# Kernel tuning notes

Measured on AMD Instinct MI355X. Metric: run time of the kernel, lower is better.

Reference implementation:

```python
import jax, jax.numpy as jnp
import numpy as np

B, I, J, C = 1, 256, 256, 128
H, D = 4, 32          # no_heads, head_dim; c_hidden = H*D = 128
INF = 1.0e9
LN_EPS = 1e-5


def setup_inputs() -> dict:
    key = jax.random.key(0)
    ks = jax.random.split(key, 8)
    x = jax.random.normal(ks[0], (B, I, J, C), dtype=jnp.float32)
    mask = (jax.random.uniform(ks[1], (B, I, J)) > 0.1).astype(jnp.float32)
    std = 0.02
    wq = std * jax.random.normal(ks[2], (H * D, C), dtype=jnp.float32)
    wk = std * jax.random.normal(ks[3], (H * D, C), dtype=jnp.float32)
    wv = std * jax.random.normal(ks[4], (H * D, C), dtype=jnp.float32)
    wb = std * jax.random.normal(ks[5], (H, C), dtype=jnp.float32)
    wo = (std / np.sqrt(2 * H)) * jax.random.normal(ks[6], (C, H * D), dtype=jnp.float32)
    wo_b = jnp.zeros((C,), dtype=jnp.float32)
    ln_g = jnp.ones((C,), dtype=jnp.float32)
    ln_b = jnp.zeros((C,), dtype=jnp.float32)
    return {"x": x, "mask": mask, "ln_g": ln_g, "ln_b": ln_b,
            "wq": wq, "wk": wk, "wv": wv, "wb": wb, "wo": wo, "wo_b": wo_b}


def reference(x, mask, ln_g, ln_b, wq, wk, wv, wb, wo, wo_b):
    # LayerNorm over channel dim
    mu = jnp.mean(x, axis=-1, keepdims=True)
    var = jnp.mean(jnp.square(x - mu), axis=-1, keepdims=True)
    xn = (x - mu) * jax.lax.rsqrt(var + LN_EPS) * ln_g + ln_b

    # QKV projections (torch Linear: y = x @ W^T), reshape to heads
    q = (xn @ wq.T).reshape(B, I, J, H, D)
    k = (xn @ wk.T).reshape(B, I, J, H, D)
    v = (xn @ wv.T).reshape(B, I, J, H, D)

    scale = 1.0 / np.sqrt(D)
    # attention within each row i over the J dimension: [B, I, H, Jq, Jk]
    scores = jnp.einsum('biqhd,bikhd->bihqk', q, k) * scale

    # triangle bias: [B, I, J, H] -> [B, I, H, Jq, 1], broadcast over keys
    tb = jnp.einsum('bijc,hc->bijh', xn, wb)
    scores = scores + jnp.swapaxes(tb, -1, -2)[..., None]

    # mask bias: inf*(mask-1) -> [B, I, 1, Jq, 1] (as in the torch code)
    scores = scores + (INF * (mask - 1.0))[:, :, None, :, None]

    attn = jax.nn.softmax(scores, axis=-1)
    out = jnp.einsum('bihqk,bikhd->biqhd', attn, v).reshape(B, I, J, H * D)
    return out @ wo.T + wo_b
```

## Files before the change

### kernel.cpp

```cpp
#include <hip/hip_runtime.h>
#include <hip/hip_bf16.h>

typedef short bf16x8 __attribute__((ext_vector_type(8)));
typedef short bf16x4 __attribute__((ext_vector_type(4)));
typedef float f32x4  __attribute__((ext_vector_type(4)));

#define NI 256
#define NJ 256
#define NC 128
#define NH 4
#define ND 32

#define WB_OFF    0
#define WO_BF_OFF 98304
#define XN_OFF    131072
#define TBM_OFF   16908288
#define OG_OFF    17956864

__device__ __forceinline__ short f2bf(float f) {
    return __builtin_bit_cast(short, __float2bfloat16(f));
}

typedef __attribute__((address_space(1))) const void gvoid_t;
typedef __attribute__((address_space(3))) void svoid_t;
__device__ __forceinline__ void load_lds16(const void* g, void* l) {
    __builtin_amdgcn_global_load_lds((gvoid_t*)g, (svoid_t*)l, 16, 0, 0);
}

__global__ __launch_bounds__(256, 8)
void k_conv(const float* __restrict__ wq, const float* __restrict__ wk,
            const float* __restrict__ wv, const float* __restrict__ wo,
            char* __restrict__ ws)
{
    const int gt = blockIdx.x * 256 + threadIdx.x;
    const int base = gt * 4;
    const float* src;
    short* dst;
    if (base < 49152) {
        const int t = base >> 14;
        src = (t == 0 ? wq : (t == 1 ? wk : wv)) + (base & 16383);
        dst = (short*)(ws + WB_OFF) + base;
    } else {
        src = wo + (base - 49152);
        dst = (short*)(ws + WO_BF_OFF) + (base - 49152);
    }
    f32x4 v = *(const f32x4*)src;
    bf16x4 o;
    #pragma unroll
    for (int r = 0; r < 4; ++r) o[r] = f2bf(v[r]);
    *(bf16x4*)dst = o;
}

__global__ __launch_bounds__(512, 4)
void k_ln(const float* __restrict__ x, const float* __restrict__ mask,
          const float* __restrict__ ln_g, const float* __restrict__ ln_b,
          const float* __restrict__ wb, char* __restrict__ ws)
{
    const int tid = threadIdx.x;
    const int t   = tid >> 2;
    const int p   = tid & 3;
    const int ch  = p * 32;
    const size_t tok = (size_t)blockIdx.x * 128 + t;

    const float* xr = x + tok * NC + ch;
    f32x4 vx[8];
    float s0 = 0.f;
    #pragma unroll
    for (int u = 0; u < 8; ++u) {
        vx[u] = *(const f32x4*)(xr + 4 * u);
        s0 += vx[u][0] + vx[u][1] + vx[u][2] + vx[u][3];
    }
    s0 += __shfl_xor(s0, 1);
    s0 += __shfl_xor(s0, 2);
    const float mu = s0 * 0.0078125f;
    float v0 = 0.f;
    #pragma unroll
    for (int u = 0; u < 8; ++u) {
        #pragma unroll
        for (int e = 0; e < 4; ++e) { float d = vx[u][e] - mu; v0 += d * d; }
    }
    v0 += __shfl_xor(v0, 1);
    v0 += __shfl_xor(v0, 2);
    const float rs = rsqrtf(v0 * 0.0078125f + 1e-5f);
    #pragma unroll
    for (int u = 0; u < 8; ++u) {
        f32x4 gg = *(const f32x4*)(ln_g + ch + 4 * u);
        f32x4 bb = *(const f32x4*)(ln_b + ch + 4 * u);
        #pragma unroll
        for (int e = 0; e < 4; ++e) vx[u][e] = (vx[u][e] - mu) * rs * gg[e] + bb[e];
    }

    float tb[4];
    #pragma unroll
    for (int h = 0; h < 4; ++h) {
        const float* wr = wb + h * NC + ch;
        float a = 0.f;
        #pragma unroll
        for (int u = 0; u < 8; ++u) {
            f32x4 w4 = *(const f32x4*)(wr + 4 * u);
            #pragma unroll
            for (int e = 0; e < 4; ++e) a += vx[u][e] * w4[e];
        }
        a += __shfl_xor(a, 1);
        a += __shfl_xor(a, 2);
        tb[h] = a;
    }
    if (p == 0) {
        const float mb = 1.0e9f * (mask[tok] - 1.0f);
        const size_t i = tok >> 8, j = tok & 255;
        float* tbm = (float*)(ws + TBM_OFF);
        #pragma unroll
        for (int h = 0; h < 4; ++h)
            tbm[(i * NH + h) * NJ + j] = tb[h] + mb;
    }

    short* xnrow = (short*)(ws + XN_OFF) + tok * NC + ch;
    #pragma unroll
    for (int cc = 0; cc < 4; ++cc) {
        bf16x8 o8;
        #pragma unroll
        for (int e = 0; e < 4; ++e) {
            o8[e]     = f2bf(vx[2 * cc][e]);
            o8[4 + e] = f2bf(vx[2 * cc + 1][e]);
        }
        *(bf16x8*)(xnrow + 8 * cc) = o8;
    }
}

__global__ __launch_bounds__(512, 4)
void k_fat(char* __restrict__ ws)
{
    __shared__ short kls[256][40];
    __shared__ short vls[32][264];
    __shared__ short pbuf[8][3][16][40];

    const int tid  = threadIdx.x;
    const int lane = tid & 63;
    const int wid  = tid >> 6;
    const int g    = lane >> 4;
    const int l16  = lane & 15;
    const int ih   = blockIdx.x;
    const int i    = ih >> 2;
    const int h    = ih & 3;

    const short* xn   = (const short*)(ws + XN_OFF) + (size_t)i * NJ * NC;
    const short* wqkv = (const short*)(ws + WB_OFF);
    const float* tbm  = (const float*)(ws + TBM_OFF) + (size_t)ih * NJ;
    short* og = (short*)(ws + OG_OFF) + ((size_t)h * (NI * NJ) + (size_t)i * NJ) * ND;

    const f32x4 z4 = {0.f, 0.f, 0.f, 0.f};

    #pragma unroll
    for (int tile = 0; tile < 2; ++tile) {
        const int tq = wid * 32 + tile * 16;
        bf16x8 af[4];
        #pragma unroll
        for (int ks = 0; ks < 4; ++ks)
            af[ks] = *(const bf16x8*)(xn + (size_t)(tq + l16) * NC + ks * 32 + g * 8);
        #pragma unroll
        for (int op = 0; op < 3; ++op) {
            #pragma unroll
            for (int sub = 0; sub < 2; ++sub) {
                const short* wrow = wqkv + (size_t)(op * 128 + h * 32 + sub * 16 + l16) * NC + g * 8;
                f32x4 acc = z4;
                #pragma unroll
                for (int ks = 0; ks < 4; ++ks) {
                    bf16x8 bf = *(const bf16x8*)(wrow + ks * 32);
                    acc = __builtin_amdgcn_mfma_f32_16x16x32_bf16(af[ks], bf, acc, 0, 0, 0);
                }
                if (op == 0) {
                    #pragma unroll
                    for (int r = 0; r < 4; ++r)
                        pbuf[wid][tile][g * 4 + r][sub * 16 + l16] = f2bf(acc[r]);
                } else if (op == 1) {
                    #pragma unroll
                    for (int r = 0; r < 4; ++r)
                        kls[tq + g * 4 + r][sub * 16 + l16] = f2bf(acc[r]);
                } else {
                    bf16x4 pk;
                    #pragma unroll
                    for (int r = 0; r < 4; ++r) pk[r] = f2bf(acc[r]);
                    *(bf16x4*)(&vls[sub * 16 + l16][tq + g * 4]) = pk;
                }
            }
        }
    }
    __syncthreads();

    const float SCALE = 0.17677669529663687f;

    #pragma unroll
    for (int qt = 0; qt < 2; ++qt) {
        const int tq = wid * 32 + qt * 16;
        f32x4 tbmb = *(const f32x4*)(tbm + tq + g * 4);

        bf16x8 qf = *(const bf16x8*)(&pbuf[wid][qt][l16][g * 8]);
        f32x4 s[16];
        #pragma unroll
        for (int kt = 0; kt < 16; ++kt) {
            bf16x8 kf = *(const bf16x8*)(&kls[kt * 16 + l16][g * 8]);
            s[kt] = __builtin_amdgcn_mfma_f32_16x16x32_bf16(qf, kf, z4, 0, 0, 0);
        }
        #pragma unroll
        for (int kt = 0; kt < 16; ++kt)
            #pragma unroll
            for (int r = 0; r < 4; ++r)
                s[kt][r] = fmaf(s[kt][r], SCALE, tbmb[r]);

        f32x4 mx = s[0];
        #pragma unroll
        for (int kt = 1; kt < 16; ++kt)
            #pragma unroll
            for (int r = 0; r < 4; ++r) mx[r] = fmaxf(mx[r], s[kt][r]);
        #pragma unroll
        for (int d = 1; d < 16; d <<= 1)
            #pragma unroll
            for (int r = 0; r < 4; ++r) mx[r] = fmaxf(mx[r], __shfl_xor(mx[r], d));

        f32x4 sum = z4;
        #pragma unroll
        for (int kt = 0; kt < 16; ++kt)
            #pragma unroll
            for (int r = 0; r < 4; ++r) { s[kt][r] = __expf(s[kt][r] - mx[r]); sum[r] += s[kt][r]; }
        #pragma unroll
        for (int d = 1; d < 16; d <<= 1)
            #pragma unroll
            for (int r = 0; r < 4; ++r) sum[r] += __shfl_xor(sum[r], d);
        f32x4 inv;
        #pragma unroll
        for (int r = 0; r < 4; ++r) inv[r] = 1.0f / sum[r];
        #pragma unroll
        for (int kt = 0; kt < 16; ++kt)
            #pragma unroll
            for (int r = 0; r < 4; ++r) s[kt][r] *= inv[r];

        f32x4 oacc0 = z4, oacc1 = z4;
        #pragma unroll
        for (int c = 0; c < 8; ++c) {
            short* pb = &pbuf[wid][(c & 1) ? 0 : 2][0][0];
            #pragma unroll
            for (int kk = 0; kk < 2; ++kk) {
                #pragma unroll
                for (int r = 0; r < 4; ++r)
                    pb[(g * 4 + r) * 40 + kk * 16 + l16] = f2bf(s[c * 2 + kk][r]);
            }
            bf16x8 a   = *(const bf16x8*)(pb + l16 * 40 + g * 8);
            bf16x8 vb0 = *(const bf16x8*)(&vls[l16][c * 32 + g * 8]);
            bf16x8 vb1 = *(const bf16x8*)(&vls[16 + l16][c * 32 + g * 8]);
            oacc0 = __builtin_amdgcn_mfma_f32_16x16x32_bf16(a, vb0, oacc0, 0, 0, 0);
            oacc1 = __builtin_amdgcn_mfma_f32_16x16x32_bf16(a, vb1, oacc1, 0, 0, 0);
        }

        #pragma unroll
        for (int r = 0; r < 4; ++r) {
            const int tok = tq + g * 4 + r;
            og[(size_t)tok * ND + l16]      = f2bf(oacc0[r]);
            og[(size_t)tok * ND + 16 + l16] = f2bf(oacc1[r]);
        }
    }
}

__global__ __launch_bounds__(512, 4)
void k_oproj(const char* __restrict__ ws, const float* __restrict__ wo_b,
             float* __restrict__ out)
{
    __shared__ short ol[4][128][32];

    const int tid  = threadIdx.x;
    const int lane = tid & 63;
    const int wid  = tid >> 6;
    const int g    = lane >> 4;
    const int l16  = lane & 15;
    const size_t tok0 = (size_t)blockIdx.x * 128;

    const short* ogb = (const short*)(ws + OG_OFF);
    for (int c = wid; c < 32; c += 8) {
        const int hh = c >> 3, cc = c & 7;
        const char* src = (const char*)(ogb + ((size_t)hh * (NI * NJ) + tok0) * ND) + cc * 1024 + lane * 16;
        load_lds16(src, (char*)ol + c * 1024);
    }
    __syncthreads();

    const short* wrow = (const short*)(ws + WO_BF_OFF) + (size_t)(wid * 16 + l16) * NC + g * 8;
    bf16x8 bfr[4];
    #pragma unroll
    for (int ks = 0; ks < 4; ++ks) bfr[ks] = *(const bf16x8*)(wrow + ks * 32);

    const float bias = wo_b[wid * 16 + l16];
    const f32x4 z4 = {0.f, 0.f, 0.f, 0.f};

    #pragma unroll
    for (int mt = 0; mt < 8; ++mt) {
        f32x4 acc = z4;
        #pragma unroll
        for (int ks = 0; ks < 4; ++ks) {
            bf16x8 av = *(const bf16x8*)(&ol[ks][mt * 16 + l16][g * 8]);
            acc = __builtin_amdgcn_mfma_f32_16x16x32_bf16(av, bfr[ks], acc, 0, 0, 0);
        }
        #pragma unroll
        for (int r = 0; r < 4; ++r)
            out[(tok0 + mt * 16 + g * 4 + r) * NC + wid * 16 + l16] = acc[r] + bias;
    }
}

extern "C" void kernel_launch(void* const* d_in, const int* in_sizes, int n_in,
                              void* d_out, int out_size, void* d_ws, size_t ws_size,
                              hipStream_t stream) {
    const float* x    = (const float*)d_in[0];
    const float* mask = (const float*)d_in[1];
    const float* ln_g = (const float*)d_in[2];
    const float* ln_b = (const float*)d_in[3];
    const float* wq   = (const float*)d_in[4];
    const float* wk   = (const float*)d_in[5];
    const float* wv   = (const float*)d_in[6];
    const float* wb   = (const float*)d_in[7];
    const float* wo   = (const float*)d_in[8];
    const float* wo_b = (const float*)d_in[9];
    float* out = (float*)d_out;
    char* ws   = (char*)d_ws;

    k_conv <<<dim3(64),     dim3(256), 0, stream>>>(wq, wk, wv, wo, ws);
    k_ln   <<<dim3(512),    dim3(512), 0, stream>>>(x, mask, ln_g, ln_b, wb, ws);
    k_fat  <<<dim3(NI * NH), dim3(512), 0, stream>>>(ws);
    k_oproj<<<dim3(512),    dim3(512), 0, stream>>>(ws, wo_b, out);
}
```

Before: 107.1 us.

## Fuse weight conversion into LN kernel, shuffle-based P/Q fragments, direct-load oproj

Merges the weight conversion and LayerNorm kernels into one launch, with extra blocks converting weights. In the attention kernel, Q is computed transposed and S is computed as K·Qᵀ, so the softmax reduction becomes per-lane with only two cross-lane shuffles. The probability and Q fragments are repacked through wave shuffles instead of an LDS staging buffer. The output projection now loads its operands directly from global memory instead of through LDS and runs with smaller 256-thread blocks, each wave computing 32 output columns. These changes aim to cut launch overhead, LDS traffic and shuffle-heavy reductions, at the cost of extra shuffle instructions and uncached global loads.

Measured after the change: 121.1 us. +13.0%, slower.

```diff
diff --git a/kernel.cpp b/kernel.cpp
--- a/kernel.cpp
+++ b/kernel.cpp
@@ -21,46 +21,65 @@
     return __builtin_bit_cast(short, __float2bfloat16(f));
 }
 
-typedef __attribute__((address_space(1))) const void gvoid_t;
-typedef __attribute__((address_space(3))) void svoid_t;
-__device__ __forceinline__ void load_lds16(const void* g, void* l) {
-    __builtin_amdgcn_global_load_lds((gvoid_t*)g, (svoid_t*)l, 16, 0, 0);
+__device__ __forceinline__ bf16x8 xchg(f32x4 pe, f32x4 po, int gg, int ll) {
+    union P { int d; short s[2]; };
+    P e0, e1, o0, o1;
+    e0.s[0] = f2bf(pe[0]); e0.s[1] = f2bf(pe[1]);
+    e1.s[0] = f2bf(pe[2]); e1.s[1] = f2bf(pe[3]);
+    o0.s[0] = f2bf(po[0]); o0.s[1] = f2bf(po[1]);
+    o1.s[0] = f2bf(po[2]); o1.s[1] = f2bf(po[3]);
+    const int sA = ((gg & 1) * 2) * 16 + ll;
+    const int sB = sA + 16;
+    const bool hi = gg >= 2;
+    int t0e = __shfl(e0.d, sA), t0o = __shfl(o0.d, sA);
+    int t1e = __shfl(e1.d, sA), t1o = __shfl(o1.d, sA);
+    int t2e = __shfl(e0.d, sB), t2o = __shfl(o0.d, sB);
+    int t3e = __shfl(e1.d, sB), t3o = __shfl(o1.d, sB);
+    union U { int d[4]; bf16x8 v; } u;
+    u.d[0] = hi ? t0o : t0e;
+    u.d[1] = hi ? t1o : t1e;
+    u.d[2] = hi ? t2o : t2e;
+    u.d[3] = hi ? t3o : t3e;
+    return u.v;
 }
 
 __global__ __launch_bounds__(256, 8)
-void k_conv(const float* __restrict__ wq, const float* __restrict__ wk,
-            const float* __restrict__ wv, const float* __restrict__ wo,
-            char* __restrict__ ws)
+void k_pre(const float* __restrict__ x, const float* __restrict__ mask,
+           const float* __restrict__ ln_g, const float* __restrict__ ln_b,
+           const float* __restrict__ wb, const float* __restrict__ wq,
+           const float* __restrict__ wk, const float* __restrict__ wv,
+           const float* __restrict__ wo, char* __restrict__ ws)
 {
-    const int gt = blockIdx.x * 256 + threadIdx.x;
-    const int base = gt * 4;
-    const float* src;
-    short* dst;
-    if (base < 49152) {
-        const int t = base >> 14;
-        src = (t == 0 ? wq : (t == 1 ? wk : wv)) + (base & 16383);
-        dst = (short*)(ws + WB_OFF) + base;
-    } else {
-        src = wo + (base - 49152);
-        dst = (short*)(ws + WO_BF_OFF) + (base - 49152);
-    }
-    f32x4 v = *(const f32x4*)src;
-    bf16x4 o;
-    #pragma unroll
-    for (int r = 0; r < 4; ++r) o[r] = f2bf(v[r]);
-    *(bf16x4*)dst = o;
-}
-
-__global__ __launch_bounds__(512, 4)
-void k_ln(const float* __restrict__ x, const float* __restrict__ mask,
-          const float* __restrict__ ln_g, const float* __restrict__ ln_b,
-          const float* __restrict__ wb, char* __restrict__ ws)
-{
+    const int bid = blockIdx.x;
     const int tid = threadIdx.x;
+
+    if (bid >= 1024) {
+        const int base = ((bid - 1024) * 256 + tid) * 8;
+        const float* src;
+        short* dst;
+        if (base < 49152) {
+            const int t = base >> 14;
+            src = (t == 0 ? wq : (t == 1 ? wk : wv)) + (base & 16383);
+            dst = (short*)(ws + WB_OFF) + base;
+        } else {
+            src = wo + (base - 49152);
+            dst = (short*)(ws + WO_BF_OFF) + (base - 49152);
+        }
+        #pragma unroll
+        for (int u = 0; u < 2; ++u) {
+            f32x4 v = *(const f32x4*)(src + 4 * u);
+            bf16x4 o;
+            #pragma unroll
+            for (int r = 0; r < 4; ++r) o[r] = f2bf(v[r]);
+            *(bf16x4*)(dst + 4 * u) = o;
+        }
+        return;
+    }
+
     const int t   = tid >> 2;
     const int p   = tid & 3;
     const int ch  = p * 32;
-    const size_t tok = (size_t)blockIdx.x * 128 + t;
+    const size_t tok = (size_t)bid * 64 + t;
 
     const float* xr = x + tok * NC + ch;
     f32x4 vx[8];
@@ -132,7 +151,6 @@
 {
     __shared__ short kls[256][40];
     __shared__ short vls[32][264];
-    __shared__ short pbuf[8][3][16][40];
 
     const int tid  = threadIdx.x;
     const int lane = tid & 63;
@@ -149,6 +167,7 @@
     short* og = (short*)(ws + OG_OFF) + ((size_t)h * (NI * NJ) + (size_t)i * NJ) * ND;
 
     const f32x4 z4 = {0.f, 0.f, 0.f, 0.f};
+    bf16x8 qf[2];
 
     #pragma unroll
     for (int tile = 0; tile < 2; ++tile) {
@@ -157,32 +176,42 @@
         #pragma unroll
         for (int ks = 0; ks < 4; ++ks)
             af[ks] = *(const bf16x8*)(xn + (size_t)(tq + l16) * NC + ks * 32 + g * 8);
-        #pragma unroll
-        for (int op = 0; op < 3; ++op) {
-            #pragma unroll
-            for (int sub = 0; sub < 2; ++sub) {
-                const short* wrow = wqkv + (size_t)(op * 128 + h * 32 + sub * 16 + l16) * NC + g * 8;
-                f32x4 acc = z4;
-                #pragma unroll
-                for (int ks = 0; ks < 4; ++ks) {
-                    bf16x8 bf = *(const bf16x8*)(wrow + ks * 32);
-                    acc = __builtin_amdgcn_mfma_f32_16x16x32_bf16(af[ks], bf, acc, 0, 0, 0);
-                }
-                if (op == 0) {
-                    #pragma unroll
-                    for (int r = 0; r < 4; ++r)
-                        pbuf[wid][tile][g * 4 + r][sub * 16 + l16] = f2bf(acc[r]);
-                } else if (op == 1) {
-                    #pragma unroll
-                    for (int r = 0; r < 4; ++r)
-                        kls[tq + g * 4 + r][sub * 16 + l16] = f2bf(acc[r]);
-                } else {
-                    bf16x4 pk;
-                    #pragma unroll
-                    for (int r = 0; r < 4; ++r) pk[r] = f2bf(acc[r]);
-                    *(bf16x4*)(&vls[sub * 16 + l16][tq + g * 4]) = pk;
-                }
+
+        {
+            f32x4 ae = z4, ao = z4;
+            #pragma unroll
+            for (int ks = 0; ks < 4; ++ks) {
+                bf16x8 w0 = *(const bf16x8*)(wqkv + (size_t)(h * 32 + l16) * NC + ks * 32 + g * 8);
+                bf16x8 w1 = *(const bf16x8*)(wqkv + (size_t)(h * 32 + 16 + l16) * NC + ks * 32 + g * 8);
+                ae = __builtin_amdgcn_mfma_f32_16x16x32_bf16(w0, af[ks], ae, 0, 0, 0);
+                ao = __builtin_amdgcn_mfma_f32_16x16x32_bf16(w1, af[ks], ao, 0, 0, 0);
             }
+            qf[tile] = xchg(ae, ao, g, l16);
+        }
+        #pragma unroll
+        for (int sub = 0; sub < 2; ++sub) {
+            f32x4 acc = z4;
+            #pragma unroll
+            for (int ks = 0; ks < 4; ++ks) {
+                bf16x8 w = *(const bf16x8*)(wqkv + (size_t)(128 + h * 32 + sub * 16 + l16) * NC + ks * 32 + g * 8);
+                acc = __builtin_amdgcn_mfma_f32_16x16x32_bf16(af[ks], w, acc, 0, 0, 0);
+            }
+            #pragma unroll
+            for (int r = 0; r < 4; ++r)
+                kls[tq + g * 4 + r][sub * 16 + l16] = f2bf(acc[r]);
+        }
+        #pragma unroll
+        for (int sub = 0; sub < 2; ++sub) {
+            f32x4 acc = z4;
+            #pragma unroll
+            for (int ks = 0; ks < 4; ++ks) {
+                bf16x8 w = *(const bf16x8*)(wqkv + (size_t)(256 + h * 32 + sub * 16 + l16) * NC + ks * 32 + g * 8);
+                acc = __builtin_amdgcn_mfma_f32_16x16x32_bf16(af[ks], w, acc, 0, 0, 0);
+            }
+            bf16x4 pk;
+            #pragma unroll
+            for (int r = 0; r < 4; ++r) pk[r] = f2bf(acc[r]);
+            *(bf16x4*)(&vls[sub * 16 + l16][tq + g * 4]) = pk;
         }
     }
     __syncthreads();
@@ -192,114 +221,103 @@
     #pragma unroll
     for (int qt = 0; qt < 2; ++qt) {
         const int tq = wid * 32 + qt * 16;
-        f32x4 tbmb = *(const f32x4*)(tbm + tq + g * 4);
-
-        bf16x8 qf = *(const bf16x8*)(&pbuf[wid][qt][l16][g * 8]);
+        const float tbq = tbm[tq + l16];
+
         f32x4 s[16];
         #pragma unroll
         for (int kt = 0; kt < 16; ++kt) {
             bf16x8 kf = *(const bf16x8*)(&kls[kt * 16 + l16][g * 8]);
-            s[kt] = __builtin_amdgcn_mfma_f32_16x16x32_bf16(qf, kf, z4, 0, 0, 0);
+            s[kt] = __builtin_amdgcn_mfma_f32_16x16x32_bf16(kf, qf[qt], z4, 0, 0, 0);
         }
         #pragma unroll
         for (int kt = 0; kt < 16; ++kt)
             #pragma unroll
             for (int r = 0; r < 4; ++r)
-                s[kt][r] = fmaf(s[kt][r], SCALE, tbmb[r]);
-
-        f32x4 mx = s[0];
-        #pragma unroll
-        for (int kt = 1; kt < 16; ++kt)
-            #pragma unroll
-            for (int r = 0; r < 4; ++r) mx[r] = fmaxf(mx[r], s[kt][r]);
-        #pragma unroll
-        for (int d = 1; d < 16; d <<= 1)
-            #pragma unroll
-            for (int r = 0; r < 4; ++r) mx[r] = fmaxf(mx[r], __shfl_xor(mx[r], d));
-
-        f32x4 sum = z4;
+                s[kt][r] = fmaf(s[kt][r], SCALE, tbq);
+
+        float m = s[0][0];
         #pragma unroll
         for (int kt = 0; kt < 16; ++kt)
             #pragma unroll
-            for (int r = 0; r < 4; ++r) { s[kt][r] = __expf(s[kt][r] - mx[r]); sum[r] += s[kt][r]; }
-        #pragma unroll
-        for (int d = 1; d < 16; d <<= 1)
-            #pragma unroll
-            for (int r = 0; r < 4; ++r) sum[r] += __shfl_xor(sum[r], d);
-        f32x4 inv;
-        #pragma unroll
-        for (int r = 0; r < 4; ++r) inv[r] = 1.0f / sum[r];
+            for (int r = 0; r < 4; ++r) m = fmaxf(m, s[kt][r]);
+        m = fmaxf(m, __shfl_xor(m, 16));
+        m = fmaxf(m, __shfl_xor(m, 32));
+
+        float sum = 0.f;
         #pragma unroll
         for (int kt = 0; kt < 16; ++kt)
             #pragma unroll
-            for (int r = 0; r < 4; ++r) s[kt][r] *= inv[r];
-
-        f32x4 oacc0 = z4, oacc1 = z4;
+            for (int r = 0; r < 4; ++r) { s[kt][r] = __expf(s[kt][r] - m); sum += s[kt][r]; }
+        sum += __shfl_xor(sum, 16);
+        sum += __shfl_xor(sum, 32);
+        const float inv = 1.0f / sum;
+        #pragma unroll
+        for (int kt = 0; kt < 16; ++kt)
+            #pragma unroll
+            for (int r = 0; r < 4; ++r) s[kt][r] *= inv;
+
+        f32x4 o0 = z4, o1 = z4;
         #pragma unroll
         for (int c = 0; c < 8; ++c) {
-            short* pb = &pbuf[wid][(c & 1) ? 0 : 2][0][0];
-            #pragma unroll
-            for (int kk = 0; kk < 2; ++kk) {
-                #pragma unroll
-                for (int r = 0; r < 4; ++r)
-                    pb[(g * 4 + r) * 40 + kk * 16 + l16] = f2bf(s[c * 2 + kk][r]);
-            }
-            bf16x8 a   = *(const bf16x8*)(pb + l16 * 40 + g * 8);
+            bf16x8 pa  = xchg(s[2 * c], s[2 * c + 1], g, l16);
             bf16x8 vb0 = *(const bf16x8*)(&vls[l16][c * 32 + g * 8]);
             bf16x8 vb1 = *(const bf16x8*)(&vls[16 + l16][c * 32 + g * 8]);
-            oacc0 = __builtin_amdgcn_mfma_f32_16x16x32_bf16(a, vb0, oacc0, 0, 0, 0);
-            oacc1 = __builtin_amdgcn_mfma_f32_16x16x32_bf16(a, vb1, oacc1, 0, 0, 0);
+            o0 = __builtin_amdgcn_mfma_f32_16x16x32_bf16(pa, vb0, o0, 0, 0, 0);
+            o1 = __builtin_amdgcn_mfma_f32_16x16x32_bf16(pa, vb1, o1, 0, 0, 0);
         }
 
         #pragma unroll
         for (int r = 0; r < 4; ++r) {
             const int tok = tq + g * 4 + r;
-            og[(size_t)tok * ND + l16]      = f2bf(oacc0[r]);
-            og[(size_t)tok * ND + 16 + l16] = f2bf(oacc1[r]);
-        }
-    }
-}
-
-__global__ __launch_bounds__(512, 4)
+            og[(size_t)tok * ND + l16]      = f2bf(o0[r]);
+            og[(size_t)tok * ND + 16 + l16] = f2bf(o1[r]);
+        }
+    }
+}
+
+__global__ __launch_bounds__(256, 4)
 void k_oproj(const char* __restrict__ ws, const float* __restrict__ wo_b,
              float* __restrict__ out)
 {
-    __shared__ short ol[4][128][32];
-
     const int tid  = threadIdx.x;
     const int lane = tid & 63;
     const int wid  = tid >> 6;
     const int g    = lane >> 4;
     const int l16  = lane & 15;
-    const size_t tok0 = (size_t)blockIdx.x * 128;
+    const size_t tok0 = (size_t)blockIdx.x * 64;
 
     const short* ogb = (const short*)(ws + OG_OFF);
-    for (int c = wid; c < 32; c += 8) {
-        const int hh = c >> 3, cc = c & 7;
-        const char* src = (const char*)(ogb + ((size_t)hh * (NI * NJ) + tok0) * ND) + cc * 1024 + lane * 16;
-        load_lds16(src, (char*)ol + c * 1024);
-    }
-    __syncthreads();
-
-    const short* wrow = (const short*)(ws + WO_BF_OFF) + (size_t)(wid * 16 + l16) * NC + g * 8;
-    bf16x8 bfr[4];
-    #pragma unroll
-    for (int ks = 0; ks < 4; ++ks) bfr[ks] = *(const bf16x8*)(wrow + ks * 32);
-
-    const float bias = wo_b[wid * 16 + l16];
+    const short* wob = (const short*)(ws + WO_BF_OFF);
     const f32x4 z4 = {0.f, 0.f, 0.f, 0.f};
 
-    #pragma unroll
-    for (int mt = 0; mt < 8; ++mt) {
-        f32x4 acc = z4;
+    bf16x8 bfr[2][4];
+    #pragma unroll
+    for (int s = 0; s < 2; ++s)
+        #pragma unroll
+        for (int ks = 0; ks < 4; ++ks)
+            bfr[s][ks] = *(const bf16x8*)(wob + (size_t)(wid * 32 + s * 16 + l16) * NC + ks * 32 + g * 8);
+
+    const float bias0 = wo_b[wid * 32 + l16];
+    const float bias1 = wo_b[wid * 32 + 16 + l16];
+
+    #pragma unroll
+    for (int mt = 0; mt < 4; ++mt) {
+        bf16x8 av[4];
+        #pragma unroll
+        for (int ks = 0; ks < 4; ++ks)
+            av[ks] = *(const bf16x8*)(ogb + ((size_t)ks * (NI * NJ) + tok0 + mt * 16 + l16) * ND + g * 8);
+        f32x4 a0 = z4, a1 = z4;
         #pragma unroll
         for (int ks = 0; ks < 4; ++ks) {
-            bf16x8 av = *(const bf16x8*)(&ol[ks][mt * 16 + l16][g * 8]);
-            acc = __builtin_amdgcn_mfma_f32_16x16x32_bf16(av, bfr[ks], acc, 0, 0, 0);
-        }
-        #pragma unroll
-        for (int r = 0; r < 4; ++r)
-            out[(tok0 + mt * 16 + g * 4 + r) * NC + wid * 16 + l16] = acc[r] + bias;
+            a0 = __builtin_amdgcn_mfma_f32_16x16x32_bf16(av[ks], bfr[0][ks], a0, 0, 0, 0);
+            a1 = __builtin_amdgcn_mfma_f32_16x16x32_bf16(av[ks], bfr[1][ks], a1, 0, 0, 0);
+        }
+        #pragma unroll
+        for (int r = 0; r < 4; ++r) {
+            const size_t row = (tok0 + mt * 16 + g * 4 + r) * NC;
+            out[row + wid * 32 + l16]      = a0[r] + bias0;
+            out[row + wid * 32 + 16 + l16] = a1[r] + bias1;
+        }
     }
 }
 
@@ -319,8 +337,7 @@
     float* out = (float*)d_out;
     char* ws   = (char*)d_ws;
 
-    k_conv <<<dim3(64),     dim3(256), 0, stream>>>(wq, wk, wv, wo, ws);
-    k_ln   <<<dim3(512),    dim3(512), 0, stream>>>(x, mask, ln_g, ln_b, wb, ws);
+    k_pre  <<<dim3(1056),   dim3(256), 0, stream>>>(x, mask, ln_g, ln_b, wb, wq, wk, wv, wo, ws);
     k_fat  <<<dim3(NI * NH), dim3(512), 0, stream>>>(ws);
-    k_oproj<<<dim3(512),    dim3(512), 0, stream>>>(ws, wo_b, out);
-}
+    k_oproj<<<dim3(1024),   dim3(256), 0, stream>>>(ws, wo_b, out);
+}
```

## Fuse output projection into attention kernel and restructure LayerNorm prep

Applied to the files above, without the earlier changes.

Merges the attention and output-projection kernels into one kernel per row i with 1024 threads, looping over the four heads and keeping the per-head outputs in LDS, so the bf16 attention output no longer makes a round trip through global memory. LayerNorm is rewritten as one wave per two tokens using a single-pass sum and sum-of-squares, and the triangle bias is folded algebraically using precomputed g·wb and b·wb terms. Weight conversion is merged with that precompute into a single prep kernel. The costs are fewer blocks (256), more barriers per block, a large dynamic LDS allocation, a less stable variance formula, and an unused stub kernel left in the source.

Measured after the change: 114.9 us. 1.07x slower.

```diff
diff --git a/kernel.cpp b/kernel.cpp
--- a/kernel.cpp
+++ b/kernel.cpp
@@ -13,188 +13,249 @@
 
 #define WB_OFF    0
 #define WO_BF_OFF 98304
-#define XN_OFF    131072
-#define TBM_OFF   16908288
-#define OG_OFF    17956864
+#define GB_OFF    131072
+#define XN_OFF    131584
+#define TBM_OFF   16908800
 
 __device__ __forceinline__ short f2bf(float f) {
     return __builtin_bit_cast(short, __float2bfloat16(f));
 }
 
-typedef __attribute__((address_space(1))) const void gvoid_t;
-typedef __attribute__((address_space(3))) void svoid_t;
-__device__ __forceinline__ void load_lds16(const void* g, void* l) {
-    __builtin_amdgcn_global_load_lds((gvoid_t*)g, (svoid_t*)l, 16, 0, 0);
-}
-
 __global__ __launch_bounds__(256, 8)
-void k_conv(const float* __restrict__ wq, const float* __restrict__ wk,
+void k_prep(const float* __restrict__ wq, const float* __restrict__ wk,
             const float* __restrict__ wv, const float* __restrict__ wo,
-            char* __restrict__ ws)
+            const float* __restrict__ ln_g, const float* __restrict__ ln_b,
+            const float* __restrict__ wb, char* __restrict__ ws)
 {
-    const int gt = blockIdx.x * 256 + threadIdx.x;
-    const int base = gt * 4;
-    const float* src;
-    short* dst;
-    if (base < 49152) {
-        const int t = base >> 14;
-        src = (t == 0 ? wq : (t == 1 ? wk : wv)) + (base & 16383);
-        dst = (short*)(ws + WB_OFF) + base;
-    } else {
-        src = wo + (base - 49152);
-        dst = (short*)(ws + WO_BF_OFF) + (base - 49152);
-    }
-    f32x4 v = *(const f32x4*)src;
-    bf16x4 o;
-    #pragma unroll
-    for (int r = 0; r < 4; ++r) o[r] = f2bf(v[r]);
-    *(bf16x4*)dst = o;
-}
-
-__global__ __launch_bounds__(512, 4)
-void k_ln(const float* __restrict__ x, const float* __restrict__ mask,
-          const float* __restrict__ ln_g, const float* __restrict__ ln_b,
-          const float* __restrict__ wb, char* __restrict__ ws)
+    const int bid = blockIdx.x;
+    const int tid = threadIdx.x;
+    if (bid < 32) {
+        const int base = (bid * 256 + tid) * 8;
+        const float* src;
+        short* dst;
+        if (base < 49152) {
+            const int t = base >> 14;
+            src = (t == 0 ? wq : (t == 1 ? wk : wv)) + (base & 16383);
+            dst = (short*)(ws + WB_OFF) + base;
+        } else {
+            src = wo + (base - 49152);
+            dst = (short*)(ws + WO_BF_OFF) + (base - 49152);
+        }
+        #pragma unroll
+        for (int u = 0; u < 2; ++u) {
+            f32x4 v = *(const f32x4*)(src + 4 * u);
+            bf16x4 o;
+            #pragma unroll
+            for (int r = 0; r < 4; ++r) o[r] = f2bf(v[r]);
+            *(bf16x4*)(dst + 4 * u) = o;
+        }
+    } else if (tid < 64) {
+        float G[4] = {0.f, 0.f, 0.f, 0.f}, Bv[4] = {0.f, 0.f, 0.f, 0.f};
+        #pragma unroll
+        for (int u = 0; u < 2; ++u) {
+            const int c = tid * 2 + u;
+            const float gc = ln_g[c], bc = ln_b[c];
+            #pragma unroll
+            for (int h = 0; h < 4; ++h) {
+                const float w = wb[h * NC + c];
+                G[h] += gc * w; Bv[h] += bc * w;
+            }
+        }
+        #pragma unroll
+        for (int dd = 1; dd < 64; dd <<= 1) {
+            #pragma unroll
+            for (int h = 0; h < 4; ++h) {
+                G[h]  += __shfl_xor(G[h], dd);
+                Bv[h] += __shfl_xor(Bv[h], dd);
+            }
+        }
+        if (tid == 0) {
+            float* GB = (float*)(ws + GB_OFF);
+            #pragma unroll
+            for (int h = 0; h < 4; ++h) { GB[h] = G[h]; GB[4 + h] = Bv[h]; }
+        }
+    }
+}
+
+__global__ __launch_bounds__(256, 8)
+void k_pre(const float* __restrict__ x, const float* __restrict__ mask,
+           const float* __restrict__ ln_g, const float* __restrict__ ln_b,
+           char* __restrict__ ws)
 {
-    const int tid = threadIdx.x;
-    const int t   = tid >> 2;
-    const int p   = tid & 3;
-    const int ch  = p * 32;
-    const size_t tok = (size_t)blockIdx.x * 128 + t;
-
-    const float* xr = x + tok * NC + ch;
-    f32x4 vx[8];
-    float s0 = 0.f;
-    #pragma unroll
-    for (int u = 0; u < 8; ++u) {
-        vx[u] = *(const f32x4*)(xr + 4 * u);
-        s0 += vx[u][0] + vx[u][1] + vx[u][2] + vx[u][3];
-    }
-    s0 += __shfl_xor(s0, 1);
-    s0 += __shfl_xor(s0, 2);
-    const float mu = s0 * 0.0078125f;
-    float v0 = 0.f;
-    #pragma unroll
-    for (int u = 0; u < 8; ++u) {
-        #pragma unroll
-        for (int e = 0; e < 4; ++e) { float d = vx[u][e] - mu; v0 += d * d; }
-    }
-    v0 += __shfl_xor(v0, 1);
-    v0 += __shfl_xor(v0, 2);
-    const float rs = rsqrtf(v0 * 0.0078125f + 1e-5f);
-    #pragma unroll
-    for (int u = 0; u < 8; ++u) {
-        f32x4 gg = *(const f32x4*)(ln_g + ch + 4 * u);
-        f32x4 bb = *(const f32x4*)(ln_b + ch + 4 * u);
-        #pragma unroll
-        for (int e = 0; e < 4; ++e) vx[u][e] = (vx[u][e] - mu) * rs * gg[e] + bb[e];
-    }
-
-    float tb[4];
+    const int tid  = threadIdx.x;
+    const int lane = tid & 63;
+    const int wv   = tid >> 6;
+    const int l5   = lane & 31;
+    const int half = lane >> 5;
+    const int c0   = l5 * 4;
+
+    f32x4 gv = *(const f32x4*)(ln_g + c0);
+    f32x4 bv = *(const f32x4*)(ln_b + c0);
+    const float* GB = (const float*)(ws + GB_OFF);
+    float Gh[4], Bh[4];
+    f32x4 gwv[4];
     #pragma unroll
     for (int h = 0; h < 4; ++h) {
-        const float* wr = wb + h * NC + ch;
-        float a = 0.f;
-        #pragma unroll
-        for (int u = 0; u < 8; ++u) {
-            f32x4 w4 = *(const f32x4*)(wr + 4 * u);
-            #pragma unroll
-            for (int e = 0; e < 4; ++e) a += vx[u][e] * w4[e];
-        }
-        a += __shfl_xor(a, 1);
-        a += __shfl_xor(a, 2);
-        tb[h] = a;
-    }
-    if (p == 0) {
-        const float mb = 1.0e9f * (mask[tok] - 1.0f);
-        const size_t i = tok >> 8, j = tok & 255;
-        float* tbm = (float*)(ws + TBM_OFF);
-        #pragma unroll
-        for (int h = 0; h < 4; ++h)
-            tbm[(i * NH + h) * NJ + j] = tb[h] + mb;
-    }
-
-    short* xnrow = (short*)(ws + XN_OFF) + tok * NC + ch;
-    #pragma unroll
-    for (int cc = 0; cc < 4; ++cc) {
-        bf16x8 o8;
-        #pragma unroll
-        for (int e = 0; e < 4; ++e) {
-            o8[e]     = f2bf(vx[2 * cc][e]);
-            o8[4 + e] = f2bf(vx[2 * cc + 1][e]);
-        }
-        *(bf16x8*)(xnrow + 8 * cc) = o8;
-    }
-}
-
-__global__ __launch_bounds__(512, 4)
-void k_fat(char* __restrict__ ws)
+        Gh[h] = GB[h]; Bh[h] = GB[4 + h];
+        f32x4 w = *(const f32x4*)((const float*)nullptr + 0);
+        (void)w;
+    }
+    const float* wbp = nullptr; (void)wbp;
+    short* xnb = (short*)(ws + XN_OFF);
+    float* tbm = (float*)(ws + TBM_OFF);
+
+    const int t0 = blockIdx.x * 64 + wv * 16;
+    (void)t0; (void)xnb; (void)tbm; (void)gv; (void)bv; (void)gwv; (void)half; (void)c0;
+}
+
+__global__ __launch_bounds__(256, 8)
+void k_pre2(const float* __restrict__ x, const float* __restrict__ mask,
+            const float* __restrict__ ln_g, const float* __restrict__ ln_b,
+            const float* __restrict__ wb, char* __restrict__ ws)
 {
-    __shared__ short kls[256][40];
-    __shared__ short vls[32][264];
-    __shared__ short pbuf[8][3][16][40];
+    const int tid  = threadIdx.x;
+    const int lane = tid & 63;
+    const int wv   = tid >> 6;
+    const int l5   = lane & 31;
+    const int half = lane >> 5;
+    const int c0   = l5 * 4;
+
+    f32x4 gv = *(const f32x4*)(ln_g + c0);
+    f32x4 bv = *(const f32x4*)(ln_b + c0);
+    f32x4 gwv[4];
+    #pragma unroll
+    for (int h = 0; h < 4; ++h) {
+        f32x4 w = *(const f32x4*)(wb + h * NC + c0);
+        #pragma unroll
+        for (int e = 0; e < 4; ++e) gwv[h][e] = gv[e] * w[e];
+    }
+    const float* GB = (const float*)(ws + GB_OFF);
+    float Gh[4], Bh[4];
+    #pragma unroll
+    for (int h = 0; h < 4; ++h) { Gh[h] = GB[h]; Bh[h] = GB[4 + h]; }
+
+    short* xnb = (short*)(ws + XN_OFF);
+    float* tbm = (float*)(ws + TBM_OFF);
+    const int t0 = blockIdx.x * 64 + wv * 16;
+
+    #pragma unroll
+    for (int it = 0; it < 2; ++it) {
+        const int tb8 = t0 + it * 8;
+        const float* bp = x + (size_t)tb8 * NC;
+        #pragma unroll
+        for (int k = 0; k < 4; ++k) {
+            f32x4 v = *(const f32x4*)(bp + k * 256 + lane * 4);
+            const int tk = tb8 + k * 2 + half;
+            float s  = v[0] + v[1] + v[2] + v[3];
+            float s2 = v[0]*v[0] + v[1]*v[1] + v[2]*v[2] + v[3]*v[3];
+            float d0 = v[0]*gwv[0][0] + v[1]*gwv[0][1] + v[2]*gwv[0][2] + v[3]*gwv[0][3];
+            float d1 = v[0]*gwv[1][0] + v[1]*gwv[1][1] + v[2]*gwv[1][2] + v[3]*gwv[1][3];
+            float d2 = v[0]*gwv[2][0] + v[1]*gwv[2][1] + v[2]*gwv[2][2] + v[3]*gwv[2][3];
+            float d3 = v[0]*gwv[3][0] + v[1]*gwv[3][1] + v[2]*gwv[3][2] + v[3]*gwv[3][3];
+            #pragma unroll
+            for (int dd = 1; dd < 32; dd <<= 1) {
+                s  += __shfl_xor(s, dd);
+                s2 += __shfl_xor(s2, dd);
+                d0 += __shfl_xor(d0, dd);
+                d1 += __shfl_xor(d1, dd);
+                d2 += __shfl_xor(d2, dd);
+                d3 += __shfl_xor(d3, dd);
+            }
+            const float mu  = s * 0.0078125f;
+            const float var = s2 * 0.0078125f - mu * mu;
+            const float rs  = rsqrtf(var + 1e-5f);
+            bf16x4 o;
+            #pragma unroll
+            for (int e = 0; e < 4; ++e) o[e] = f2bf((v[e] - mu) * rs * gv[e] + bv[e]);
+            *(bf16x4*)(xnb + (size_t)tk * NC + c0) = o;
+            if (l5 == 0) {
+                const float mb = 1.0e9f * (mask[tk] - 1.0f);
+                const int ii = tk >> 8, jj = tk & 255;
+                const float d4[4] = {d0, d1, d2, d3};
+                #pragma unroll
+                for (int h = 0; h < 4; ++h)
+                    tbm[(size_t)(ii * NH + h) * NJ + jj] = rs * (d4[h] - mu * Gh[h]) + Bh[h] + mb;
+            }
+        }
+    }
+}
+
+#define SMEM_FAT 147968
+__global__ __launch_bounds__(1024, 4)
+void k_fat2(const char* __restrict__ ws, const float* __restrict__ wo_b,
+            float* __restrict__ out)
+{
+    extern __shared__ __align__(16) char smem[];
+    short (*kls)[40]  = (short(*)[40])(smem);
+    short (*vls)[264] = (short(*)[264])(smem + 20480);
+    short (*ols)[136] = (short(*)[136])(smem + 78336);
 
     const int tid  = threadIdx.x;
     const int lane = tid & 63;
     const int wid  = tid >> 6;
     const int g    = lane >> 4;
     const int l16  = lane & 15;
-    const int ih   = blockIdx.x;
-    const int i    = ih >> 2;
-    const int h    = ih & 3;
+    const int i    = blockIdx.x;
+    const int tq   = wid * 16;
+
+    short* qsl = (short*)(smem + 37376) + wid * 1280;
 
     const short* xn   = (const short*)(ws + XN_OFF) + (size_t)i * NJ * NC;
     const short* wqkv = (const short*)(ws + WB_OFF);
-    const float* tbm  = (const float*)(ws + TBM_OFF) + (size_t)ih * NJ;
-    short* og = (short*)(ws + OG_OFF) + ((size_t)h * (NI * NJ) + (size_t)i * NJ) * ND;
+    const short* wob  = (const short*)(ws + WO_BF_OFF);
+    const float* tbmB = (const float*)(ws + TBM_OFF) + (size_t)i * NH * NJ;
 
     const f32x4 z4 = {0.f, 0.f, 0.f, 0.f};
-
-    #pragma unroll
-    for (int tile = 0; tile < 2; ++tile) {
-        const int tq = wid * 32 + tile * 16;
+    const float SCALE = 0.17677669529663687f;
+
+    for (int h = 0; h < NH; ++h) {
         bf16x8 af[4];
         #pragma unroll
         for (int ks = 0; ks < 4; ++ks)
             af[ks] = *(const bf16x8*)(xn + (size_t)(tq + l16) * NC + ks * 32 + g * 8);
         #pragma unroll
-        for (int op = 0; op < 3; ++op) {
-            #pragma unroll
-            for (int sub = 0; sub < 2; ++sub) {
-                const short* wrow = wqkv + (size_t)(op * 128 + h * 32 + sub * 16 + l16) * NC + g * 8;
-                f32x4 acc = z4;
-                #pragma unroll
-                for (int ks = 0; ks < 4; ++ks) {
-                    bf16x8 bf = *(const bf16x8*)(wrow + ks * 32);
-                    acc = __builtin_amdgcn_mfma_f32_16x16x32_bf16(af[ks], bf, acc, 0, 0, 0);
-                }
-                if (op == 0) {
-                    #pragma unroll
-                    for (int r = 0; r < 4; ++r)
-                        pbuf[wid][tile][g * 4 + r][sub * 16 + l16] = f2bf(acc[r]);
-                } else if (op == 1) {
-                    #pragma unroll
-                    for (int r = 0; r < 4; ++r)
-                        kls[tq + g * 4 + r][sub * 16 + l16] = f2bf(acc[r]);
-                } else {
-                    bf16x4 pk;
-                    #pragma unroll
-                    for (int r = 0; r < 4; ++r) pk[r] = f2bf(acc[r]);
-                    *(bf16x4*)(&vls[sub * 16 + l16][tq + g * 4]) = pk;
-                }
-            }
-        }
-    }
-    __syncthreads();
-
-    const float SCALE = 0.17677669529663687f;
-
-    #pragma unroll
-    for (int qt = 0; qt < 2; ++qt) {
-        const int tq = wid * 32 + qt * 16;
+        for (int sub = 0; sub < 2; ++sub) {
+            f32x4 acc = z4;
+            #pragma unroll
+            for (int ks = 0; ks < 4; ++ks) {
+                bf16x8 w = *(const bf16x8*)(wqkv + (size_t)(h * 32 + sub * 16 + l16) * NC + ks * 32 + g * 8);
+                acc = __builtin_amdgcn_mfma_f32_16x16x32_bf16(af[ks], w, acc, 0, 0, 0);
+            }
+            #pragma unroll
+            for (int r = 0; r < 4; ++r)
+                qsl[(g * 4 + r) * 40 + sub * 16 + l16] = f2bf(acc[r]);
+        }
+        #pragma unroll
+        for (int sub = 0; sub < 2; ++sub) {
+            f32x4 acc = z4;
+            #pragma unroll
+            for (int ks = 0; ks < 4; ++ks) {
+                bf16x8 w = *(const bf16x8*)(wqkv + (size_t)(128 + h * 32 + sub * 16 + l16) * NC + ks * 32 + g * 8);
+                acc = __builtin_amdgcn_mfma_f32_16x16x32_bf16(af[ks], w, acc, 0, 0, 0);
+            }
+            #pragma unroll
+            for (int r = 0; r < 4; ++r)
+                kls[tq + g * 4 + r][sub * 16 + l16] = f2bf(acc[r]);
+        }
+        #pragma unroll
+        for (int sub = 0; sub < 2; ++sub) {
+            f32x4 acc = z4;
+            #pragma unroll
+            for (int ks = 0; ks < 4; ++ks) {
+                bf16x8 w = *(const bf16x8*)(wqkv + (size_t)(256 + h * 32 + sub * 16 + l16) * NC + ks * 32 + g * 8);
+                acc = __builtin_amdgcn_mfma_f32_16x16x32_bf16(af[ks], w, acc, 0, 0, 0);
+            }
+            bf16x4 pk;
+            #pragma unroll
+            for (int r = 0; r < 4; ++r) pk[r] = f2bf(acc[r]);
+            *(bf16x4*)(&vls[sub * 16 + l16][tq + g * 4]) = pk;
+        }
+        __syncthreads();
+
+        const float* tbm = tbmB + (size_t)h * NJ;
         f32x4 tbmb = *(const f32x4*)(tbm + tq + g * 4);
-
-        bf16x8 qf = *(const bf16x8*)(&pbuf[wid][qt][l16][g * 8]);
+        bf16x8 qf = *(const bf16x8*)(qsl + l16 * 40 + g * 8);
+
         f32x4 s[16];
         #pragma unroll
         for (int kt = 0; kt < 16; ++kt) {
@@ -234,10 +295,10 @@
             #pragma unroll
             for (int r = 0; r < 4; ++r) s[kt][r] *= inv[r];
 
-        f32x4 oacc0 = z4, oacc1 = z4;
+        f32x4 o0 = z4, o1 = z4;
         #pragma unroll
         for (int c = 0; c < 8; ++c) {
-            short* pb = &pbuf[wid][(c & 1) ? 0 : 2][0][0];
+            short* pb = qsl + (c & 1) * 640;
             #pragma unroll
             for (int kk = 0; kk < 2; ++kk) {
                 #pragma unroll
@@ -247,59 +308,36 @@
             bf16x8 a   = *(const bf16x8*)(pb + l16 * 40 + g * 8);
             bf16x8 vb0 = *(const bf16x8*)(&vls[l16][c * 32 + g * 8]);
             bf16x8 vb1 = *(const bf16x8*)(&vls[16 + l16][c * 32 + g * 8]);
-            oacc0 = __builtin_amdgcn_mfma_f32_16x16x32_bf16(a, vb0, oacc0, 0, 0, 0);
-            oacc1 = __builtin_amdgcn_mfma_f32_16x16x32_bf16(a, vb1, oacc1, 0, 0, 0);
+            o0 = __builtin_amdgcn_mfma_f32_16x16x32_bf16(a, vb0, o0, 0, 0, 0);
+            o1 = __builtin_amdgcn_mfma_f32_16x16x32_bf16(a, vb1, o1, 0, 0, 0);
         }
 
         #pragma unroll
         for (int r = 0; r < 4; ++r) {
-            const int tok = tq + g * 4 + r;
-            og[(size_t)tok * ND + l16]      = f2bf(oacc0[r]);
-            og[(size_t)tok * ND + 16 + l16] = f2bf(oacc1[r]);
-        }
-    }
-}
-
-__global__ __launch_bounds__(512, 4)
-void k_oproj(const char* __restrict__ ws, const float* __restrict__ wo_b,
-             float* __restrict__ out)
-{
-    __shared__ short ol[4][128][32];
-
-    const int tid  = threadIdx.x;
-    const int lane = tid & 63;
-    const int wid  = tid >> 6;
-    const int g    = lane >> 4;
-    const int l16  = lane & 15;
-    const size_t tok0 = (size_t)blockIdx.x * 128;
-
-    const short* ogb = (const short*)(ws + OG_OFF);
-    for (int c = wid; c < 32; c += 8) {
-        const int hh = c >> 3, cc = c & 7;
-        const char* src = (const char*)(ogb + ((size_t)hh * (NI * NJ) + tok0) * ND) + cc * 1024 + lane * 16;
-        load_lds16(src, (char*)ol + c * 1024);
-    }
-    __syncthreads();
-
-    const short* wrow = (const short*)(ws + WO_BF_OFF) + (size_t)(wid * 16 + l16) * NC + g * 8;
-    bf16x8 bfr[4];
-    #pragma unroll
-    for (int ks = 0; ks < 4; ++ks) bfr[ks] = *(const bf16x8*)(wrow + ks * 32);
-
-    const float bias = wo_b[wid * 16 + l16];
-    const f32x4 z4 = {0.f, 0.f, 0.f, 0.f};
-
-    #pragma unroll
-    for (int mt = 0; mt < 8; ++mt) {
+            ols[tq + g * 4 + r][h * 32 + l16]      = f2bf(o0[r]);
+            ols[tq + g * 4 + r][h * 32 + 16 + l16] = f2bf(o1[r]);
+        }
+        __syncthreads();
+    }
+
+    bf16x8 oaf[4];
+    #pragma unroll
+    for (int ks = 0; ks < 4; ++ks)
+        oaf[ks] = *(const bf16x8*)(&ols[tq + l16][ks * 32 + g * 8]);
+    #pragma unroll
+    for (int ct = 0; ct < 8; ++ct) {
+        bf16x8 bfr[4];
+        #pragma unroll
+        for (int ks = 0; ks < 4; ++ks)
+            bfr[ks] = *(const bf16x8*)(wob + (size_t)(ct * 16 + l16) * NC + ks * 32 + g * 8);
         f32x4 acc = z4;
         #pragma unroll
-        for (int ks = 0; ks < 4; ++ks) {
-            bf16x8 av = *(const bf16x8*)(&ol[ks][mt * 16 + l16][g * 8]);
-            acc = __builtin_amdgcn_mfma_f32_16x16x32_bf16(av, bfr[ks], acc, 0, 0, 0);
-        }
+        for (int ks = 0; ks < 4; ++ks)
+            acc = __builtin_amdgcn_mfma_f32_16x16x32_bf16(oaf[ks], bfr[ks], acc, 0, 0, 0);
+        const float bias = wo_b[ct * 16 + l16];
         #pragma unroll
         for (int r = 0; r < 4; ++r)
-            out[(tok0 + mt * 16 + g * 4 + r) * NC + wid * 16 + l16] = acc[r] + bias;
+            out[((size_t)i * NJ + tq + g * 4 + r) * NC + ct * 16 + l16] = acc[r] + bias;
     }
 }
 
@@ -319,8 +357,10 @@
     float* out = (float*)d_out;
     char* ws   = (char*)d_ws;
 
-    k_conv <<<dim3(64),     dim3(256), 0, stream>>>(wq, wk, wv, wo, ws);
-    k_ln   <<<dim3(512),    dim3(512), 0, stream>>>(x, mask, ln_g, ln_b, wb, ws);
-    k_fat  <<<dim3(NI * NH), dim3(512), 0, stream>>>(ws);
-    k_oproj<<<dim3(512),    dim3(512), 0, stream>>>(ws, wo_b, out);
-}
+    (void)hipFuncSetAttribute((const void*)k_fat2,
+                              hipFuncAttributeMaxDynamicSharedMemorySize, SMEM_FAT);
+
+    k_prep<<<dim3(33),   dim3(256), 0, stream>>>(wq, wk, wv, wo, ln_g, ln_b, wb, ws);
+    k_pre2<<<dim3(1024), dim3(256), 0, stream>>>(x, mask, ln_g, ln_b, wb, ws);
+    k_fat2<<<dim3(256),  dim3(1024), SMEM_FAT, stream>>>(ws, wo_b, out);
+}
```
